# Kernel optimization log

Measured on AMD Instinct MI355X. Metric: run time of the kernel, lower is better.

Reference implementation:

```python
import jax, jax.numpy as jnp
import numpy as np

B, S, D, P, W = 16, 100, 8192, 100, 3  # batch, seq, feat dim, proj width, window size


def setup_inputs() -> dict:
    key = jax.random.key(0)
    ks = jax.random.split(key, 6)
    return {
        "x": jax.random.normal(ks[0], (B, S, D), dtype=jnp.float32),
        "wq": jax.random.normal(ks[1], (D, P), dtype=jnp.float32) * (1.0 / np.sqrt(D)),
        "wk": jax.random.normal(ks[2], (D, P), dtype=jnp.float32) * (1.0 / np.sqrt(D)),
        "wv": jax.random.normal(ks[3], (D, P), dtype=jnp.float32) * (1.0 / np.sqrt(D)),
        "forwardpad": jax.random.normal(ks[4], (B, 1, D), dtype=jnp.float32),
        "backwardpad": jax.random.normal(ks[5], (B, 1, D), dtype=jnp.float32),
    }


def reference(x, wq, wk, wv, forwardpad, backwardpad):
    # pad: (B, S+2, D)
    padded = jnp.concatenate([forwardpad, x, backwardpad], axis=1)
    # gather all 100 overlapping size-3 windows at once: (B, S, W, D)
    idx = jnp.arange(S)[:, None] + jnp.arange(W)[None, :]  # (S, W)
    windows = padded[:, idx, :]
    # shared projections across all windows (original recomputed per window)
    q = jnp.einsum("bswd,dp->bswp", windows, wq)
    k = jnp.einsum("bswd,dp->bswp", windows, wk)
    v = jnp.einsum("bswd,dp->bswp", windows, wv)
    # per-window 3x3 attention
    scores = jnp.einsum("bswp,bsup->bswu", q, k)  # (B, S, W, W)
    attn = jax.nn.softmax(scores, axis=-1)
    out = jnp.einsum("bswu,bsup->bswp", attn, v)  # (B, S, W, P)
    # original concatenates windows along seq then takes [:, 1::3, :] -> center token of each window
    return out[:, :, 1, :]  # (B, S, P)
```

## Files before the change

kernel.cpp:

```cpp
#include <hip/hip_runtime.h>
#include <hip/hip_bf16.h>
#include <hip/hip_fp16.h>

constexpr int Dk   = 8192;
constexpr int Bb   = 16;
constexpr int Ss   = 100;
constexpr int Pp   = 100;
constexpr int MROW = 1632;
constexpr int NT   = 20;
constexpr int NCC  = 320;
constexpr int NQ   = 304;
constexpr int KG   = 1024;
constexpr int KC   = 32;
constexpr int CH   = 5;
constexpr int MBL2 = 26;

constexpr size_t B_SEG   = (size_t)NT * KG * 128;
constexpr size_t PSTRIDE = (size_t)1664 * NCC;

typedef short s8v __attribute__((ext_vector_type(8)));
typedef short s4v __attribute__((ext_vector_type(4)));
typedef float f4v __attribute__((ext_vector_type(4)));

__device__ inline unsigned short f2bf_rne(float f) {
    unsigned u = __float_as_uint(f);
    u += 0x7fffu + ((u >> 16) & 1u);
    return (unsigned short)(u >> 16);
}

__global__ __launch_bounds__(256) void pack_b(
    const float* __restrict__ wq, const float* __restrict__ wk,
    const float* __restrict__ wv,
    short* __restrict__ b_hi, short* __restrict__ b_lo) {
    const int id = blockIdx.x * 256 + threadIdx.x;
    const int n  = id % NCC;
    const int kg = id / NCC;
    if (kg >= KG) return;

    const float* w = nullptr; int p = 0;
    if (n < 100)      { w = wq; p = n; }
    else if (n < 200) { w = wk; p = n - 100; }
    else if (n < 300) { w = wv; p = n - 200; }

    s8v hi, lo;
    #pragma unroll
    for (int j = 0; j < 8; ++j) {
        const float v = w ? w[(size_t)(kg * 8 + j) * Pp + p] : 0.0f;
        const unsigned u = __float_as_uint(v);
        hi[j] = (short)(unsigned short)(u >> 16);
        const float hf = __uint_as_float(u & 0xffff0000u);
        lo[j] = (short)f2bf_rne(v - hf);
    }
    const size_t doff = ((size_t)(n >> 4) * KG + kg) * 128 + (size_t)(n & 15) * 8;
    *(s8v*)(b_hi + doff) = hi;
    *(s8v*)(b_lo + doff) = lo;
}

__global__ __launch_bounds__(256, 2) void qkv_gemm(
    const float* __restrict__ x, const float* __restrict__ fpad,
    const float* __restrict__ bpad,
    const short* __restrict__ b_hi, const short* __restrict__ b_lo,
    unsigned short* __restrict__ part) {
    __shared__ __align__(16) short ahis[2][2048];
    __shared__ __align__(16) short alos[2][2048];

    const int id   = blockIdx.x;
    const int xcd  = id & 7;
    const int slot = id >> 3;
    const int sub  = slot / MBL2;
    const int kc   = xcd * 4 + sub;
    const int mb   = slot - sub * MBL2;

    const int tid  = threadIdx.x;
    const int w    = tid >> 6;
    const int l    = tid & 63;
    const int m    = l & 15;
    const int quad = l >> 4;

    const int sr  = tid >> 2;
    const int skq = tid & 3;
    const float* sp;
    {
        const int r = mb * 64 + sr;
        if (r >= MROW) sp = fpad;
        else {
            const int b = r / 102, rr = r - b * 102;
            if (rr == 0)        sp = fpad + (size_t)b * Dk;
            else if (rr == 101) sp = bpad + (size_t)b * Dk;
            else                sp = x + ((size_t)b * Ss + (rr - 1)) * Dk;
        }
        sp += kc * 256 + skq * 8;
    }
    const int woff = ((sr >> 4) * 4 + skq) * 128 + (sr & 15) * 8;

    float4 av0[2], av1[2];
    #pragma unroll
    for (int p = 0; p < 2; ++p) {
        av0[p] = *(const float4*)(sp + p * 32);
        av1[p] = *(const float4*)(sp + p * 32 + 4);
    }

    s8v bh[2][5], bl[2][5];
    {
        const int kg0 = kc * 32 + quad;
        #pragma unroll
        for (int j = 0; j < 5; ++j) {
            const size_t bo = ((size_t)(w * 5 + j) * KG + kg0) * 128 + (size_t)m * 8;
            bh[0][j] = *(const s8v*)(b_hi + bo);
            bl[0][j] = *(const s8v*)(b_lo + bo);
        }
    }

    f4v acc[4][5];
    #pragma unroll
    for (int i = 0; i < 4; ++i)
        #pragma unroll
        for (int j = 0; j < 5; ++j) {
            f4v z = {0.f, 0.f, 0.f, 0.f};
            acc[i][j] = z;
        }

    #pragma unroll
    for (int s = 0; s < 8; ++s) {
        const int cur = s & 1, nxt = cur ^ 1;

        const float4 va0 = av0[s & 1];
        const float4 va1 = av1[s & 1];

        if (s < 7) {
            const int kgn = kc * 32 + (s + 1) * 4 + quad;
            #pragma unroll
            for (int j = 0; j < 5; ++j) {
                const size_t bo = ((size_t)(w * 5 + j) * KG + kgn) * 128 + (size_t)m * 8;
                bh[nxt][j] = *(const s8v*)(b_hi + bo);
                bl[nxt][j] = *(const s8v*)(b_lo + bo);
            }
        }
        if (s < 6) {
            av0[s & 1] = *(const float4*)(sp + (s + 2) * 32);
            av1[s & 1] = *(const float4*)(sp + (s + 2) * 32 + 4);
        }

        const float vv[8] = {va0.x, va0.y, va0.z, va0.w,
                             va1.x, va1.y, va1.z, va1.w};
        s8v h8, l8;
        #pragma unroll
        for (int jj = 0; jj < 8; ++jj) {
            const unsigned u = __float_as_uint(vv[jj]);
            h8[jj] = (short)(unsigned short)(u >> 16);
            l8[jj] = (short)f2bf_rne(vv[jj] - __uint_as_float(u & 0xffff0000u));
        }

        *(s8v*)&ahis[cur][woff] = h8;
        *(s8v*)&alos[cur][woff] = l8;

        asm volatile("s_waitcnt lgkmcnt(0)\n\ts_barrier" ::: "memory");

        s8v ah[4], al[4];
        #pragma unroll
        for (int i = 0; i < 4; ++i) {
            ah[i] = *(const s8v*)&ahis[cur][((i * 4 + quad) * 16 + m) * 8];
            al[i] = *(const s8v*)&alos[cur][((i * 4 + quad) * 16 + m) * 8];
        }

        #pragma unroll
        for (int j = 0; j < 5; ++j) {
            const s8v bhv = bh[cur][j], blv = bl[cur][j];
            #pragma unroll
            for (int i = 0; i < 4; ++i)
                acc[i][j] = __builtin_amdgcn_mfma_f32_16x16x32_bf16(ah[i], bhv, acc[i][j], 0, 0, 0);
            #pragma unroll
            for (int i = 0; i < 4; ++i)
                acc[i][j] = __builtin_amdgcn_mfma_f32_16x16x32_bf16(al[i], bhv, acc[i][j], 0, 0, 0);
            #pragma unroll
            for (int i = 0; i < 4; ++i)
                acc[i][j] = __builtin_amdgcn_mfma_f32_16x16x32_bf16(ah[i], blv, acc[i][j], 0, 0, 0);
        }
    }

    unsigned short* __restrict__ pout = part + (size_t)kc * PSTRIDE;
    #pragma unroll
    for (int i = 0; i < 4; ++i) {
        #pragma unroll
        for (int j = 0; j < 5; ++j) {
            const int col  = (w * 5 + j) * 16 + m;
            const int row0 = mb * 64 + i * 16 + quad * 4;
            #pragma unroll
            for (int r = 0; r < 4; ++r)
                pout[(size_t)(row0 + r) * NCC + col] =
                    __half_as_ushort(__float2half(acc[i][j][r]));
        }
    }
}

__global__ __launch_bounds__(256) void reduce_k(
    const unsigned short* __restrict__ part, float* __restrict__ qkv) {
    const int t = blockIdx.x * 256 + threadIdx.x;
    const int row = t / 40;
    const int col0 = (t - row * 40) * 8;
    const size_t base = (size_t)row * NCC + col0;

    float sum[8] = {0.f, 0.f, 0.f, 0.f, 0.f, 0.f, 0.f, 0.f};
    #pragma unroll
    for (int k = 0; k < KC; ++k) {
        const s8v u = *(const s8v*)(part + (size_t)k * PSTRIDE + base);
        #pragma unroll
        for (int ii = 0; ii < 8; ++ii)
            sum[ii] += __half2float(__ushort_as_half((unsigned short)u[ii]));
    }
    if (col0 < NQ) {
        f4v a = {sum[0], sum[1], sum[2], sum[3]};
        f4v b = {sum[4], sum[5], sum[6], sum[7]};
        *(f4v*)(qkv + (size_t)row * NQ + col0)     = a;
        *(f4v*)(qkv + (size_t)row * NQ + col0 + 4) = b;
    }
}

__global__ __launch_bounds__(256) void attn3(
    const float* __restrict__ qkv, float* __restrict__ out) {
    const int blk = blockIdx.x;
    const int b  = blk / (Ss / CH);
    const int c  = blk % (Ss / CH);
    const int s0 = c * CH;
    const int tid = threadIdx.x;

    __shared__ float red[CH + 2][304];
    __shared__ float sc[CH][3];

    for (int idx = tid; idx < (CH + 2) * 300; idx += 256) {
        const int row = idx / 300, col = idx % 300;
        red[row][col] = qkv[(size_t)(b * 102 + s0 + row) * NQ + col];
    }
    __syncthreads();

    if (tid < CH * 3 * 16) {
        const int d = tid >> 4, g = tid & 15;
        const int ss = d / 3, u = d % 3;
        float ps = 0.0f;
        #pragma unroll
        for (int t = 0; t < 7; ++t) {
            const int p = g + t * 16;
            if (p < Pp) ps += red[ss + 1][p] * red[ss + u][100 + p];
        }
        #pragma unroll
        for (int off = 8; off > 0; off >>= 1) ps += __shfl_down(ps, off, 16);
        if (g == 0) sc[ss][u] = ps;
    }
    __syncthreads();

    for (int idx = tid; idx < CH * Pp; idx += 256) {
        const int ss = idx / Pp, p = idx % Pp;
        const float a0 = sc[ss][0], a1 = sc[ss][1], a2 = sc[ss][2];
        const float mx = fmaxf(a0, fmaxf(a1, a2));
        const float e0 = __expf(a0 - mx), e1 = __expf(a1 - mx), e2 = __expf(a2 - mx);
        const float inv = 1.0f / (e0 + e1 + e2);
        out[(size_t)(b * Ss + s0 + ss) * Pp + p] =
            inv * (e0 * red[ss][200 + p] + e1 * red[ss + 1][200 + p] +
                   e2 * red[ss + 2][200 + p]);
    }
}

extern "C" void kernel_launch(void* const* d_in, const int* in_sizes, int n_in,
                              void* d_out, int out_size, void* d_ws, size_t ws_size,
                              hipStream_t stream) {
    const float* x    = (const float*)d_in[0];
    const float* wq   = (const float*)d_in[1];
    const float* wk   = (const float*)d_in[2];
    const float* wv   = (const float*)d_in[3];
    const float* fpad = (const float*)d_in[4];
    const float* bpad = (const float*)d_in[5];
    float* out = (float*)d_out;

    short* b_hi = (short*)d_ws;
    short* b_lo = b_hi + B_SEG;
    unsigned short* part = (unsigned short*)(b_lo + B_SEG);
    float* qkv = (float*)(part + (size_t)KC * PSTRIDE);

    pack_b<<<(NCC * KG) / 256, 256, 0, stream>>>(wq, wk, wv, b_hi, b_lo);
    qkv_gemm<<<MBL2 * KC, 256, 0, stream>>>(x, fpad, bpad, b_hi, b_lo, part);
    reduce_k<<<260, 256, 0, stream>>>(part, qkv);
    attn3<<<Bb * (Ss / CH), 256, 0, stream>>>(qkv, out);
}
```

Measured before the change: 141.1 us.

## Reduce split-K to 8 chunks and stream B tiles via global_load_lds double buffering

Cuts the K-split from 32 to 8 chunks, so each block walks 32 k-steps instead of 8. This writes fewer fp16 partials and leaves less work for the reduction kernel. The B (weight hi/lo) fragments are now copied straight into a double-buffered LDS region with global_load_lds, and explicit vmcnt waits pipeline them two steps ahead. The trade-offs are about 208 blocks for 256 CUs, occupancy lowered to one block per CU, and a large LDS footprint per block.

Result: slower. 146.2 us (+3.7%).

```diff
diff --git a/kernel.cpp b/kernel.cpp
--- a/kernel.cpp
+++ b/kernel.cpp
@@ -11,7 +11,7 @@
 constexpr int NCC  = 320;
 constexpr int NQ   = 304;
 constexpr int KG   = 1024;
-constexpr int KC   = 32;
+constexpr int KC   = 8;
 constexpr int CH   = 5;
 constexpr int MBL2 = 26;
 
@@ -26,6 +26,12 @@
     unsigned u = __float_as_uint(f);
     u += 0x7fffu + ((u >> 16) & 1u);
     return (unsigned short)(u >> 16);
+}
+
+__device__ inline void gl_lds16(const short* g, short* l) {
+    __builtin_amdgcn_global_load_lds(
+        (const __attribute__((address_space(1))) void*)g,
+        (__attribute__((address_space(3))) void*)l, 16, 0, 0);
 }
 
 __global__ __launch_bounds__(256) void pack_b(
@@ -56,20 +62,18 @@
     *(s8v*)(b_lo + doff) = lo;
 }
 
-__global__ __launch_bounds__(256, 2) void qkv_gemm(
+__global__ __launch_bounds__(256, 1) void qkv_gemm(
     const float* __restrict__ x, const float* __restrict__ fpad,
     const float* __restrict__ bpad,
     const short* __restrict__ b_hi, const short* __restrict__ b_lo,
     unsigned short* __restrict__ part) {
     __shared__ __align__(16) short ahis[2][2048];
     __shared__ __align__(16) short alos[2][2048];
+    __shared__ __align__(16) short bld[2][4][5][2][512];
 
     const int id   = blockIdx.x;
-    const int xcd  = id & 7;
-    const int slot = id >> 3;
-    const int sub  = slot / MBL2;
-    const int kc   = xcd * 4 + sub;
-    const int mb   = slot - sub * MBL2;
+    const int kc   = id & 7;
+    const int mb   = id >> 3;
 
     const int tid  = threadIdx.x;
     const int w    = tid >> 6;
@@ -89,26 +93,28 @@
             else if (rr == 101) sp = bpad + (size_t)b * Dk;
             else                sp = x + ((size_t)b * Ss + (rr - 1)) * Dk;
         }
-        sp += kc * 256 + skq * 8;
+        sp += kc * 1024 + skq * 8;
     }
     const int woff = ((sr >> 4) * 4 + skq) * 128 + (sr & 15) * 8;
 
+    const short *pbh[5], *pbl[5];
+    #pragma unroll
+    for (int j = 0; j < 5; ++j) {
+        const size_t nb = ((size_t)(w * 5 + j) * KG + (size_t)kc * 128) * 128 + (size_t)l * 8;
+        pbh[j] = b_hi + nb;
+        pbl[j] = b_lo + nb;
+    }
+
     float4 av0[2], av1[2];
     #pragma unroll
-    for (int p = 0; p < 2; ++p) {
-        av0[p] = *(const float4*)(sp + p * 32);
-        av1[p] = *(const float4*)(sp + p * 32 + 4);
-    }
-
-    s8v bh[2][5], bl[2][5];
-    {
-        const int kg0 = kc * 32 + quad;
+    for (int t = 0; t < 2; ++t) {
         #pragma unroll
         for (int j = 0; j < 5; ++j) {
-            const size_t bo = ((size_t)(w * 5 + j) * KG + kg0) * 128 + (size_t)m * 8;
-            bh[0][j] = *(const s8v*)(b_hi + bo);
-            bl[0][j] = *(const s8v*)(b_lo + bo);
-        }
+            gl_lds16(pbh[j] + (size_t)t * 512, &bld[t][w][j][0][0]);
+            gl_lds16(pbl[j] + (size_t)t * 512, &bld[t][w][j][1][0]);
+        }
+        av0[t] = *(const float4*)(sp + t * 32);
+        av1[t] = *(const float4*)(sp + t * 32 + 4);
     }
 
     f4v acc[4][5];
@@ -120,63 +126,67 @@
             acc[i][j] = z;
         }
 
-    #pragma unroll
-    for (int s = 0; s < 8; ++s) {
-        const int cur = s & 1, nxt = cur ^ 1;
-
-        const float4 va0 = av0[s & 1];
-        const float4 va1 = av1[s & 1];
-
-        if (s < 7) {
-            const int kgn = kc * 32 + (s + 1) * 4 + quad;
-            #pragma unroll
-            for (int j = 0; j < 5; ++j) {
-                const size_t bo = ((size_t)(w * 5 + j) * KG + kgn) * 128 + (size_t)m * 8;
-                bh[nxt][j] = *(const s8v*)(b_hi + bo);
-                bl[nxt][j] = *(const s8v*)(b_lo + bo);
-            }
-        }
-        if (s < 6) {
-            av0[s & 1] = *(const float4*)(sp + (s + 2) * 32);
-            av1[s & 1] = *(const float4*)(sp + (s + 2) * 32 + 4);
-        }
-
-        const float vv[8] = {va0.x, va0.y, va0.z, va0.w,
-                             va1.x, va1.y, va1.z, va1.w};
-        s8v h8, l8;
-        #pragma unroll
-        for (int jj = 0; jj < 8; ++jj) {
-            const unsigned u = __float_as_uint(vv[jj]);
-            h8[jj] = (short)(unsigned short)(u >> 16);
-            l8[jj] = (short)f2bf_rne(vv[jj] - __uint_as_float(u & 0xffff0000u));
-        }
-
-        *(s8v*)&ahis[cur][woff] = h8;
-        *(s8v*)&alos[cur][woff] = l8;
-
-        asm volatile("s_waitcnt lgkmcnt(0)\n\ts_barrier" ::: "memory");
-
-        s8v ah[4], al[4];
-        #pragma unroll
-        for (int i = 0; i < 4; ++i) {
-            ah[i] = *(const s8v*)&ahis[cur][((i * 4 + quad) * 16 + m) * 8];
-            al[i] = *(const s8v*)&alos[cur][((i * 4 + quad) * 16 + m) * 8];
-        }
-
-        #pragma unroll
-        for (int j = 0; j < 5; ++j) {
-            const s8v bhv = bh[cur][j], blv = bl[cur][j];
-            #pragma unroll
-            for (int i = 0; i < 4; ++i)
-                acc[i][j] = __builtin_amdgcn_mfma_f32_16x16x32_bf16(ah[i], bhv, acc[i][j], 0, 0, 0);
-            #pragma unroll
-            for (int i = 0; i < 4; ++i)
-                acc[i][j] = __builtin_amdgcn_mfma_f32_16x16x32_bf16(al[i], bhv, acc[i][j], 0, 0, 0);
-            #pragma unroll
-            for (int i = 0; i < 4; ++i)
-                acc[i][j] = __builtin_amdgcn_mfma_f32_16x16x32_bf16(ah[i], blv, acc[i][j], 0, 0, 0);
-        }
-    }
+#define QSTEP(S, WAITSTR, DO_ISSUE)                                            \
+    {                                                                          \
+        const int cur_ = (S) & 1;                                              \
+        const float4 va0_ = av0[cur_], va1_ = av1[cur_];                       \
+        asm volatile("s_waitcnt vmcnt(" WAITSTR ")" ::: "memory");             \
+        const float vv_[8] = {va0_.x, va0_.y, va0_.z, va0_.w,                  \
+                              va1_.x, va1_.y, va1_.z, va1_.w};                 \
+        s8v h8_, l8_;                                                          \
+        _Pragma("unroll")                                                      \
+        for (int jj = 0; jj < 8; ++jj) {                                       \
+            const unsigned u_ = __float_as_uint(vv_[jj]);                      \
+            h8_[jj] = (short)(unsigned short)(u_ >> 16);                       \
+            l8_[jj] = (short)f2bf_rne(vv_[jj] - __uint_as_float(u_ & 0xffff0000u)); \
+        }                                                                      \
+        *(s8v*)&ahis[cur_][woff] = h8_;                                        \
+        *(s8v*)&alos[cur_][woff] = l8_;                                        \
+        asm volatile("s_waitcnt lgkmcnt(0)\n\ts_barrier" ::: "memory");        \
+        s8v ah_[4], al_[4], bhv_[5], blv_[5];                                  \
+        _Pragma("unroll")                                                      \
+        for (int i = 0; i < 4; ++i) {                                          \
+            ah_[i] = *(const s8v*)&ahis[cur_][((i * 4 + quad) * 16 + m) * 8];  \
+            al_[i] = *(const s8v*)&alos[cur_][((i * 4 + quad) * 16 + m) * 8];  \
+        }                                                                      \
+        _Pragma("unroll")                                                      \
+        for (int j = 0; j < 5; ++j) {                                          \
+            bhv_[j] = *(const s8v*)&bld[cur_][w][j][0][l * 8];                 \
+            blv_[j] = *(const s8v*)&bld[cur_][w][j][1][l * 8];                 \
+        }                                                                      \
+        asm volatile("s_waitcnt lgkmcnt(0)" ::: "memory");                     \
+        if (DO_ISSUE) {                                                        \
+            const int t_ = (S) + 2;                                            \
+            const int nc_ = t_ & 1;                                            \
+            const size_t ko_ = (size_t)t_ * 512;                               \
+            _Pragma("unroll")                                                  \
+            for (int j = 0; j < 5; ++j) {                                      \
+                gl_lds16(pbh[j] + ko_, &bld[nc_][w][j][0][0]);                 \
+                gl_lds16(pbl[j] + ko_, &bld[nc_][w][j][1][0]);                 \
+            }                                                                  \
+            av0[nc_] = *(const float4*)(sp + t_ * 32);                         \
+            av1[nc_] = *(const float4*)(sp + t_ * 32 + 4);                     \
+        }                                                                      \
+        _Pragma("unroll")                                                      \
+        for (int j = 0; j < 5; ++j) {                                          \
+            const s8v bh_ = bhv_[j], bl_ = blv_[j];                            \
+            _Pragma("unroll")                                                  \
+            for (int i = 0; i < 4; ++i)                                        \
+                acc[i][j] = __builtin_amdgcn_mfma_f32_16x16x32_bf16(ah_[i], bh_, acc[i][j], 0, 0, 0); \
+            _Pragma("unroll")                                                  \
+            for (int i = 0; i < 4; ++i)                                        \
+                acc[i][j] = __builtin_amdgcn_mfma_f32_16x16x32_bf16(al_[i], bh_, acc[i][j], 0, 0, 0); \
+            _Pragma("unroll")                                                  \
+            for (int i = 0; i < 4; ++i)                                        \
+                acc[i][j] = __builtin_amdgcn_mfma_f32_16x16x32_bf16(ah_[i], bl_, acc[i][j], 0, 0, 0); \
+        }                                                                      \
+    }
+
+    #pragma unroll 2
+    for (int s = 0; s < 30; ++s) QSTEP(s, "12", 1)
+    QSTEP(30, "12", 0)
+    QSTEP(31, "0", 0)
+#undef QSTEP
 
     unsigned short* __restrict__ pout = part + (size_t)kc * PSTRIDE;
     #pragma unroll
```

## Stage full A tile in LDS upfront and remap blocks so split-K slices share row tiles

Applied to the files above, without the earlier changes.

Converts the whole 64x256 A slice to hi/lo bf16 and writes it to shared memory before the MFMA loop. This replaces the per-step double-buffered conversion and the barrier inside every iteration with a single __syncthreads. It also changes the block-to-(kc, mb) mapping so that consecutive slots on an XCD share the same row block across four K chunks. The cost is 64KB of LDS per block, which may limit occupancy below the requested two blocks per CU, and the global A loads no longer overlap with compute.

Result: no change. 143.9 us (+2.0%).

```diff
diff --git a/kernel.cpp b/kernel.cpp
--- a/kernel.cpp
+++ b/kernel.cpp
@@ -19,7 +19,6 @@
 constexpr size_t PSTRIDE = (size_t)1664 * NCC;
 
 typedef short s8v __attribute__((ext_vector_type(8)));
-typedef short s4v __attribute__((ext_vector_type(4)));
 typedef float f4v __attribute__((ext_vector_type(4)));
 
 __device__ inline unsigned short f2bf_rne(float f) {
@@ -61,15 +60,15 @@
     const float* __restrict__ bpad,
     const short* __restrict__ b_hi, const short* __restrict__ b_lo,
     unsigned short* __restrict__ part) {
-    __shared__ __align__(16) short ahis[2][2048];
-    __shared__ __align__(16) short alos[2][2048];
+    __shared__ __align__(16) short ahi[16384];
+    __shared__ __align__(16) short alo[16384];
 
     const int id   = blockIdx.x;
     const int xcd  = id & 7;
     const int slot = id >> 3;
-    const int sub  = slot / MBL2;
+    const int sub  = slot & 3;
     const int kc   = xcd * 4 + sub;
-    const int mb   = slot - sub * MBL2;
+    const int mb   = slot >> 2;
 
     const int tid  = threadIdx.x;
     const int w    = tid >> 6;
@@ -91,14 +90,24 @@
         }
         sp += kc * 256 + skq * 8;
     }
-    const int woff = ((sr >> 4) * 4 + skq) * 128 + (sr & 15) * 8;
-
-    float4 av0[2], av1[2];
-    #pragma unroll
-    for (int p = 0; p < 2; ++p) {
-        av0[p] = *(const float4*)(sp + p * 32);
-        av1[p] = *(const float4*)(sp + p * 32 + 4);
-    }
+
+    #pragma unroll
+    for (int it = 0; it < 8; ++it) {
+        const float4 v0 = *(const float4*)(sp + it * 32);
+        const float4 v1 = *(const float4*)(sp + it * 32 + 4);
+        const float vv[8] = {v0.x, v0.y, v0.z, v0.w, v1.x, v1.y, v1.z, v1.w};
+        s8v h8, l8;
+        #pragma unroll
+        for (int jj = 0; jj < 8; ++jj) {
+            const unsigned u = __float_as_uint(vv[jj]);
+            h8[jj] = (short)(unsigned short)(u >> 16);
+            l8[jj] = (short)f2bf_rne(vv[jj] - __uint_as_float(u & 0xffff0000u));
+        }
+        const int off = (((sr >> 4) * 32 + it * 4 + skq) * 16 + (sr & 15)) * 8;
+        *(s8v*)&ahi[off] = h8;
+        *(s8v*)&alo[off] = l8;
+    }
+    __syncthreads();
 
     s8v bh[2][5], bl[2][5];
     {
@@ -123,9 +132,6 @@
     #pragma unroll
     for (int s = 0; s < 8; ++s) {
         const int cur = s & 1, nxt = cur ^ 1;
-
-        const float4 va0 = av0[s & 1];
-        const float4 va1 = av1[s & 1];
 
         if (s < 7) {
             const int kgn = kc * 32 + (s + 1) * 4 + quad;
@@ -136,31 +142,13 @@
                 bl[nxt][j] = *(const s8v*)(b_lo + bo);
             }
         }
-        if (s < 6) {
-            av0[s & 1] = *(const float4*)(sp + (s + 2) * 32);
-            av1[s & 1] = *(const float4*)(sp + (s + 2) * 32 + 4);
-        }
-
-        const float vv[8] = {va0.x, va0.y, va0.z, va0.w,
-                             va1.x, va1.y, va1.z, va1.w};
-        s8v h8, l8;
-        #pragma unroll
-        for (int jj = 0; jj < 8; ++jj) {
-            const unsigned u = __float_as_uint(vv[jj]);
-            h8[jj] = (short)(unsigned short)(u >> 16);
-            l8[jj] = (short)f2bf_rne(vv[jj] - __uint_as_float(u & 0xffff0000u));
-        }
-
-        *(s8v*)&ahis[cur][woff] = h8;
-        *(s8v*)&alos[cur][woff] = l8;
-
-        asm volatile("s_waitcnt lgkmcnt(0)\n\ts_barrier" ::: "memory");
 
         s8v ah[4], al[4];
         #pragma unroll
         for (int i = 0; i < 4; ++i) {
-            ah[i] = *(const s8v*)&ahis[cur][((i * 4 + quad) * 16 + m) * 8];
-            al[i] = *(const s8v*)&alos[cur][((i * 4 + quad) * 16 + m) * 8];
+            const int ao = ((i * 32 + s * 4 + quad) * 16 + m) * 8;
+            ah[i] = *(const s8v*)&ahi[ao];
+            al[i] = *(const s8v*)&alo[ao];
         }
 
         #pragma unroll
```
